# Performance work log

Measured on AMD Instinct MI355X. Metric: run time of the kernel, lower is better.

Reference implementation:

```python
import jax, jax.numpy as jnp
import numpy as np

D_MODEL = 1024
N_HEADS = 16
HEAD_DIM = D_MODEL // N_HEADS  # 64
SEQ = 2048
BATCH = 2


def setup_inputs() -> dict:
    key = jax.random.key(0)
    ks = jax.random.split(key, 12)
    s = 1.0 / np.sqrt(D_MODEL)
    return {
        "query": jax.random.normal(ks[0], (SEQ, BATCH, D_MODEL), jnp.float32),
        "key": jax.random.normal(ks[1], (SEQ, BATCH, D_MODEL), jnp.float32),
        "value": jax.random.normal(ks[2], (SEQ, BATCH, D_MODEL), jnp.float32),
        "Wq": jax.random.normal(ks[3], (D_MODEL, D_MODEL), jnp.float32) * s,
        "bq": jax.random.normal(ks[4], (D_MODEL,), jnp.float32) * s,
        "Wk": jax.random.normal(ks[5], (D_MODEL, D_MODEL), jnp.float32) * s,
        "bk": jax.random.normal(ks[6], (D_MODEL,), jnp.float32) * s,
        "Wv": jax.random.normal(ks[7], (D_MODEL, D_MODEL), jnp.float32) * s,
        "bv": jax.random.normal(ks[8], (D_MODEL,), jnp.float32) * s,
        "Wo": jax.random.normal(ks[9], (D_MODEL, D_MODEL), jnp.float32) * s,
        "bo": jax.random.normal(ks[10], (D_MODEL,), jnp.float32) * s,
    }


def _rope_tables(seq_len):
    # theta_i = 1 / 10000^(2i/head_dim), i in [0, head_dim//2)
    theta = 1.0 / (10000.0 ** (2.0 * jnp.arange(HEAD_DIM // 2, dtype=jnp.float32) / HEAD_DIM))
    pos = jnp.arange(seq_len, dtype=jnp.float32)[:, None, None, None] * theta  # [S,1,1,hd/2]
    return jnp.sin(pos), jnp.cos(pos)


def _apply_rope(t, sin, cos):
    # t: [S, B, H, hd]; NOTE faithful to source: t2 = q1*sin - q2*cos (minus)
    h = HEAD_DIM // 2
    q1, q2 = t[..., :h], t[..., h:]
    return jnp.concatenate([q1 * cos - q2 * sin, q1 * sin - q2 * cos], axis=-1)


def reference(query, key, value, Wq, bq, Wk, bk, Wv, bv, Wo, bo):
    S, B, _ = query.shape
    q = (query @ Wq.T + bq).reshape(S, B, N_HEADS, HEAD_DIM)
    k = (key @ Wk.T + bk).reshape(S, B, N_HEADS, HEAD_DIM)
    v = (value @ Wv.T + bv).reshape(S, B, N_HEADS, HEAD_DIM)
    sin, cos = _rope_tables(S)
    q = _apply_rope(q, sin, cos)
    k = _apply_rope(k, sin, cos)
    # [S,B,H,d] -> [B,H,S,d]
    q = q.transpose(1, 2, 0, 3)
    k = k.transpose(1, 2, 0, 3)
    v = v.transpose(1, 2, 0, 3)
    scale = 1.0 / jnp.sqrt(jnp.float32(HEAD_DIM))
    scores = jnp.einsum("bhqd,bhkd->bhqk", q, k) * scale
    attn = jax.nn.softmax(scores, axis=-1)
    out = jnp.einsum("bhqk,bhkd->bhqd", attn, v)  # [B,H,S,d]
    out = out.transpose(2, 0, 1, 3).reshape(S, B, D_MODEL)
    return out @ Wo.T + bo
```

## Files before the change

kernel.cpp:

```cpp
#include <hip/hip_runtime.h>
#include <hip/hip_bf16.h>

#define DMODEL 1024
#define NHEADS 16
#define HDIM   64
#define SEQ    2048
#define BATCH  2
#define MROWS  (SEQ*BATCH)

typedef unsigned int u32;
typedef unsigned short u16;
typedef __attribute__((ext_vector_type(8))) short bfrag;
typedef __attribute__((ext_vector_type(4))) float f32x4;
typedef __attribute__((ext_vector_type(16))) float f32x16;
typedef union { u32 u[4]; bfrag f; } fragu;

#define LOG2E 1.44269504088896341f

__device__ __forceinline__ u32 f2bf(float x) {
    unsigned u = __float_as_uint(x);
    return (u + 0x7fffu + ((u >> 16) & 1u)) >> 16;
}
__device__ __forceinline__ float bf2f(u32 h) {
    return __uint_as_float(h << 16);
}
__device__ __forceinline__ u32 pk2bf(float a, float b) {
    __hip_bfloat162 t = __float22bfloat162_rn(make_float2(a, b));
    u32 r;
    __builtin_memcpy(&r, &t, 4);
    return r;
}
__device__ __forceinline__ float fexp2(float x) {
#if __has_builtin(__builtin_amdgcn_exp2f)
    return __builtin_amdgcn_exp2f(x);
#else
    return exp2f(x);
#endif
}

__device__ __forceinline__ void gld16(const void* g, void* l) {
    __builtin_amdgcn_global_load_lds(
        (const __attribute__((address_space(1))) unsigned int*)g,
        (__attribute__((address_space(3))) unsigned int*)l, 16, 0, 0);
}


__global__ __launch_bounds__(256) void prep_kernel(
    const float* __restrict__ Wq, const float* __restrict__ Wk,
    const float* __restrict__ Wv, const float* __restrict__ Wo,
    float* __restrict__ query, float* __restrict__ key, float* __restrict__ value,
    u16* __restrict__ wqb, u16* __restrict__ wkb, u16* __restrict__ wvb,
    u16* __restrict__ wob, float2* __restrict__ tab)
{
    const int y = blockIdx.y;
    if (y == 3) {
        if (blockIdx.x >= 256) return;
        const int e = blockIdx.x * 256 + threadIdx.x;
        const int s = e >> 5, i = e & 31;
        const double th = exp(-(double)i * (9.210340371976184 / 32.0));
        double sn, cs;
        sincos((double)s * th, &sn, &cs);
        tab[e] = make_float2((float)sn, (float)cs);
        return;
    }
    const float* src;
    u16* dst;
    int nr;
    if (y < 3 || y == 7) {
        src = (y == 0) ? Wq : (y == 1) ? Wk : (y == 2) ? Wv : Wo;
        dst = (y == 0) ? wqb : (y == 1) ? wkb : (y == 2) ? wvb : wob;
        nr = 2;
    } else {
        float* io = (y == 4) ? query : (y == 5) ? key : value;
        src = io;
        dst = (u16*)io;
        nr = 8;
    }
    const int lane = threadIdx.x & 63;
    const int wv   = threadIdx.x >> 6;
    const int g8   = lane >> 3;
    const int l8   = lane & 7;
    for (int r = 0; r < nr; ++r) {
        const size_t kb = (size_t)blockIdx.x * (4 * nr) + (size_t)r * 4 + wv;
        const float4 x4 = *(const float4*)(src + kb * 256 + lane * 4);
        __align__(8) u16 hb[4];
        __align__(8) u16 lb[4];
        const float xs[4] = {x4.x, x4.y, x4.z, x4.w};
        #pragma unroll
        for (int i = 0; i < 4; ++i) {
            const u32 h = f2bf(xs[i]);
            hb[i] = (u16)h;
            lb[i] = (u16)f2bf(xs[i] - bf2f(h));
        }
        u16* o = dst + kb * 512 + g8 * 64 + l8 * 4;
        *(uint2*)o        = *(const uint2*)hb;
        *(uint2*)(o + 32) = *(const uint2*)lb;
    }
}

template <int NI>
__device__ __forceinline__ void gemm_body(
    int id, int mode,
    const u16* __restrict__ Ab, const u16* __restrict__ Wb,
    const float* __restrict__ bias, const float2* __restrict__ tab,
    float rope_scale,
    u16* __restrict__ Oh, u16* __restrict__ Ol, float* __restrict__ Of,
    u16* smem16)
{
    u16* sA = smem16;
    u16* sB = smem16 + 16384;

    const int tid   = threadIdx.x;
    const int w     = tid >> 6;
    const int lane  = tid & 63;
    const int lrow  = lane & 15;
    const int lquad = lane >> 4;

    const int NBLK = 1024 / (NI * 16);
    const int xcd  = id & 7;
    const int jj   = id >> 3;
    const int nblk = jj & (NBLK - 1);
    const int mblk = (xcd << 2) | (jj / NBLK);
    const int n0   = nblk * NI * 16;
    const int m0   = mblk * 128;

    const int srow8 = lane >> 3;
    const int sch   = (lane & 7) ^ srow8;

    int aoffh[2], aoffl[2], boffh[NI], boffl[NI];
    #pragma unroll
    for (int mi = 0; mi < 2; ++mi) {
        const int ra = w * 32 + mi * 16 + lrow;
        aoffh[mi] = ra * 64 + ((lquad ^ (ra & 7)) << 3);
        aoffl[mi] = ra * 64 + (((lquad + 4) ^ (ra & 7)) << 3);
    }
    #pragma unroll
    for (int ni = 0; ni < NI; ++ni) {
        const int rb = ni * 16 + lrow;
        boffh[ni] = rb * 64 + ((lquad ^ (rb & 7)) << 3);
        boffl[ni] = rb * 64 + (((lquad + 4) ^ (rb & 7)) << 3);
    }

    f32x4 acc[2][NI] = {};

    auto stage = [&](int t) {
        const int h = t & 1;
        #pragma unroll
        for (int i = 0; i < 4; ++i) {
            const int slab = w * 4 + i;
            const int row  = slab * 8 + srow8;
            gld16(Ab + (size_t)(m0 + row) * 2048 + t * 64 + sch * 8,
                  sA + h * 8192 + slab * 512);
        }
        #pragma unroll
        for (int i = 0; i < NI / 2; ++i) {
            const int slab = w * (NI / 2) + i;
            const int row  = slab * 8 + srow8;
            gld16(Wb + (size_t)(n0 + row) * 2048 + t * 64 + sch * 8,
                  sB + h * (NI * 1024) + slab * 512);
        }
    };

    stage(0);
    for (int t = 0; t < 32; ++t) {
        __syncthreads();
        if (t < 31) stage(t + 1);
        const int h = t & 1;
        const u16* sAh_ = sA + h * 8192;
        const u16* sBh_ = sB + h * (NI * 1024);

        bfrag ah[2], al[2], bh[NI], bl[NI];
        #pragma unroll
        for (int mi = 0; mi < 2; ++mi) {
            ah[mi] = *(const bfrag*)&sAh_[aoffh[mi]];
            al[mi] = *(const bfrag*)&sAh_[aoffl[mi]];
        }
        #pragma unroll
        for (int ni = 0; ni < NI; ++ni) {
            bh[ni] = *(const bfrag*)&sBh_[boffh[ni]];
            bl[ni] = *(const bfrag*)&sBh_[boffl[ni]];
        }

        #pragma unroll
        for (int mi = 0; mi < 2; ++mi)
            #pragma unroll
            for (int ni = 0; ni < NI; ++ni) {
                acc[mi][ni] = __builtin_amdgcn_mfma_f32_16x16x32_bf16(ah[mi], bh[ni], acc[mi][ni], 0, 0, 0);
                acc[mi][ni] = __builtin_amdgcn_mfma_f32_16x16x32_bf16(ah[mi], bl[ni], acc[mi][ni], 0, 0, 0);
                acc[mi][ni] = __builtin_amdgcn_mfma_f32_16x16x32_bf16(al[mi], bh[ni], acc[mi][ni], 0, 0, 0);
            }
    }

    float bn[NI];
    #pragma unroll
    for (int ni = 0; ni < NI; ++ni) bn[ni] = bias[n0 + ni * 16 + lrow];

    if (mode == 0) {
        #pragma unroll
        for (int mi = 0; mi < 2; ++mi)
            #pragma unroll
            for (int r = 0; r < 4; ++r) {
                const int mrow = w * 32 + mi * 16 + lquad * 4 + r;
                const int m  = m0 + mrow;
                const int bb = m & 1;
                const int sg = m >> 1;
                #pragma unroll
                for (int hh = 0; hh < NI / 4; ++hh) {
                    const int head = nblk * (NI / 4) + hh;
                    const size_t ob = (((size_t)(bb * NHEADS + head) * SEQ) + sg) * HDIM;
                    #pragma unroll
                    for (int ni = 0; ni < 2; ++ni) {
                        const int i = ni * 16 + lrow;
                        const float2 sc = tab[(size_t)sg * 32 + i];
                        const float x1 = acc[mi][hh * 4 + ni][r]     + bn[hh * 4 + ni];
                        const float x2 = acc[mi][hh * 4 + ni + 2][r] + bn[hh * 4 + ni + 2];
                        const float o1 = (x1 * sc.y - x2 * sc.x) * rope_scale;
                        const float o2 = (x1 * sc.x - x2 * sc.y) * rope_scale;
                        const u32 h1 = f2bf(o1);
                        const u32 h2 = f2bf(o2);
                        Oh[ob + i]      = (u16)h1;  Ol[ob + i]      = (u16)f2bf(o1 - bf2f(h1));
                        Oh[ob + i + 32] = (u16)h2;  Ol[ob + i + 32] = (u16)f2bf(o2 - bf2f(h2));
                    }
                }
            }
        return;
    }
    if (mode == 1) {
        __syncthreads();
        u32* vb = (u32*)smem16;
        constexpr int NP = (NI == 8) ? 2 : 1;
        for (int p = 0; p < NP; ++p) {
            if (p) __syncthreads();
            #pragma unroll
            for (int mi = 0; mi < 2; ++mi)
                #pragma unroll
                for (int r = 0; r < 4; ++r) {
                    const int mrow = w * 32 + mi * 16 + lquad * 4 + r;
                    const int bb = mrow & 1;
                    const int sl = mrow >> 1;
                    if (NP == 1 || bb == p) {
                        const int vbase = (NP == 1) ? bb * 4160 : 0;
                        #pragma unroll
                        for (int ni = 0; ni < NI; ++ni) {
                            const int d = ni * 16 + lrow;
                            vb[vbase + d * 65 + sl] = f2bf(acc[mi][ni][r] + bn[ni]);
                        }
                    }
                }
            __syncthreads();
            #pragma unroll
            for (int rep = 0; rep < 4; ++rep) {
                const int c  = rep * 256 + tid;
                const int bb = (NP == 1) ? (c >> 9) : p;
                const int dc = (NP == 1) ? ((c >> 3) & 63) : (c >> 3);
                const int s8 = c & 7;
                const int vbase = (NP == 1) ? bb * 4160 : 0;
                __align__(8) u16 hb[8];
                #pragma unroll
                for (int j = 0; j < 8; ++j)
                    hb[j] = (u16)vb[vbase + dc * 65 + s8 * 8 + j];
                const int head = nblk * (NI / 4) + (dc >> 6);
                const int dd   = dc & 63;
                const size_t orow = ((size_t)(bb * NHEADS + head) * HDIM + dd) * SEQ + (m0 >> 1);
                const int blk16 = (s8 >> 1) * 16;
                const int off   = (s8 & 1) * 4;
                *(uint2*)&Oh[orow + blk16 + off]     = *(const uint2*)&hb[0];
                *(uint2*)&Oh[orow + blk16 + 8 + off] = *(const uint2*)&hb[4];
            }
        }
        return;
    }
    #pragma unroll
    for (int mi = 0; mi < 2; ++mi)
        #pragma unroll
        for (int r = 0; r < 4; ++r) {
            const int m = m0 + w * 32 + mi * 16 + lquad * 4 + r;
            #pragma unroll
            for (int ni = 0; ni < NI; ++ni)
                Of[(size_t)m * 1024 + n0 + ni * 16 + lrow] = acc[mi][ni][r] + bn[ni];
        }
}

__global__ __launch_bounds__(256) void qkv_gemm_kernel(
    const u16* __restrict__ query, const u16* __restrict__ key,
    const u16* __restrict__ value,
    const u16* __restrict__ Wqb, const u16* __restrict__ Wkb,
    const u16* __restrict__ Wvb,
    const float* __restrict__ bq, const float* __restrict__ bk,
    const float* __restrict__ bv, const float2* __restrict__ tab,
    u16* __restrict__ Qh, u16* __restrict__ Ql,
    u16* __restrict__ Kh, u16* __restrict__ Kl,
    u16* __restrict__ VTh)
{
    __shared__ u16 smem16[32768];
    const int z  = blockIdx.z;
    const int id = blockIdx.x + 16 * blockIdx.y;
    const u16* A    = (z == 0) ? query : (z == 1) ? key : value;
    const u16* Wb   = (z == 0) ? Wqb : (z == 1) ? Wkb : Wvb;
    const float* bb = (z == 0) ? bq : (z == 1) ? bk : bv;
    u16* Oh = (z == 0) ? Qh : (z == 1) ? Kh : VTh;
    u16* Ol = (z == 0) ? Ql : (z == 1) ? Kl : nullptr;
    const int mode = (z == 2) ? 1 : 0;
    const float scale = (z == 0) ? 0.125f * LOG2E : 1.0f;
    gemm_body<8>(id, mode, A, Wb, bb, tab, scale, Oh, Ol, nullptr, smem16);
}

__global__ __launch_bounds__(256) void out_gemm_kernel(
    const u16* __restrict__ Ab, const u16* __restrict__ Wb,
    const float* __restrict__ bias, float* __restrict__ Of)
{
    __shared__ u16 smem16[24576];
    const int id = blockIdx.x + 16 * blockIdx.y;
    gemm_body<4>(id, 2, Ab, Wb, bias, nullptr, 1.0f, nullptr, nullptr, Of, smem16);
}

__global__ __launch_bounds__(256) void attn_mfma_kernel(
    const u16* __restrict__ Qh, const u16* __restrict__ Ql,
    const u16* __restrict__ Kh, const u16* __restrict__ Kl,
    const u16* __restrict__ Vh,
    u16* __restrict__ AOb)
{
    __shared__ u16 sKh[8192], sKl[8192];
    __shared__ u16 sVh[8192];

    const int tid  = threadIdx.x;
    const int w    = tid >> 6;
    const int lane = tid & 63;
    const int l31  = lane & 31;
    const int g    = lane >> 5;

    const int id = blockIdx.x + 16 * blockIdx.y;
    const int jj = id >> 3;
    const int bh = ((id & 7) << 2) | (jj >> 4);
    const int qt = jj & 15;

    const size_t qg = ((size_t)bh * SEQ + qt * 128 + w * 32 + l31) * HDIM + g * 8;
    bfrag qfh[4], qfl[4];
    #pragma unroll
    for (int ks = 0; ks < 4; ++ks) {
        qfh[ks] = *(const bfrag*)&Qh[qg + ks * 16];
        qfl[ks] = *(const bfrag*)&Ql[qg + ks * 16];
    }

    const int srow   = lane >> 3;
    const int schunk = (lane & 7) ^ srow;
    const u16* gsrc = nullptr; u16* lbase = nullptr; size_t istep = 0, ktstep = 0;
    if (w == 0) {
        gsrc = Kh + ((size_t)bh * SEQ + srow) * HDIM + schunk * 8;
        istep = 8 * 64; ktstep = 64 * 64; lbase = sKh;
    } else if (w == 1) {
        gsrc = Kl + ((size_t)bh * SEQ + srow) * HDIM + schunk * 8;
        istep = 8 * 64; ktstep = 64 * 64; lbase = sKl;
    } else if (w == 2) {
        gsrc = Vh + ((size_t)bh * HDIM + srow) * SEQ + schunk * 8;
        istep = 8 * SEQ; ktstep = 64; lbase = sVh;
    }

    int koff[2][4];
    #pragma unroll
    for (int a = 0; a < 2; ++a) {
        const int row = a * 32 + l31;
        #pragma unroll
        for (int c = 0; c < 4; ++c)
            koff[a][c] = row * 64 + (((c * 2 + g) ^ (row & 7)) << 3);
    }

    f32x16 accO[2] = {};
    float l_loc = 0.0f;

    auto stage = [&](int kt) {
        if (w < 3) {
            const u16* gp = gsrc + (size_t)kt * ktstep;
            u16* dst = lbase + (kt & 1) * 4096;
            #pragma unroll
            for (int i = 0; i < 8; ++i)
                gld16(gp + (size_t)i * istep, dst + i * 512);
        }
    };

    stage(0);
    for (int kt = 0; kt < SEQ / 64; ++kt) {
        __syncthreads();
        if (kt < SEQ / 64 - 1) stage(kt + 1);
        const int po = (kt & 1) * 4096;

        f32x16 accS[2] = {};
        #pragma unroll
        for (int kg = 0; kg < 2; ++kg)
            #pragma unroll
            for (int ks = 0; ks < 4; ++ks) {
                const bfrag kh_ = *(const bfrag*)&sKh[po + koff[kg][ks]];
                const bfrag kl_ = *(const bfrag*)&sKl[po + koff[kg][ks]];
                accS[kg] = __builtin_amdgcn_mfma_f32_32x32x16_bf16(kh_, qfh[ks], accS[kg], 0, 0, 0);
                accS[kg] = __builtin_amdgcn_mfma_f32_32x32x16_bf16(kh_, qfl[ks], accS[kg], 0, 0, 0);
                accS[kg] = __builtin_amdgcn_mfma_f32_32x32x16_bf16(kl_, qfh[ks], accS[kg], 0, 0, 0);
            }

        float pv[2][16];
        #pragma unroll
        for (int kg = 0; kg < 2; ++kg)
            #pragma unroll
            for (int r = 0; r < 16; ++r) {
                const float p = fexp2(accS[kg][r]);
                pv[kg][r] = p;
                l_loc += p;
            }

        #pragma unroll
        for (int kp = 0; kp < 4; ++kp) {
            const int kg = kp >> 1;
            const int t8 = (kp & 1) * 8;
            fragu ph;
            #pragma unroll
            for (int j2 = 0; j2 < 4; ++j2)
                ph.u[j2] = pk2bf(pv[kg][t8 + 2 * j2], pv[kg][t8 + 2 * j2 + 1]);
            #pragma unroll
            for (int dt = 0; dt < 2; ++dt) {
                const bfrag vh = *(const bfrag*)&sVh[po + koff[dt][kp]];
                accO[dt] = __builtin_amdgcn_mfma_f32_32x32x16_bf16(vh, ph.f, accO[dt], 0, 0, 0);
            }
        }
    }

    const float inv = 1.0f / (l_loc + __shfl_xor(l_loc, 32));

    const int b = bh >> 4;
    const int h = bh & 15;
    const int sg = qt * 128 + w * 32 + l31;
    const int rm = sg * BATCH + b;
    #pragma unroll
    for (int dt = 0; dt < 2; ++dt)
        #pragma unroll
        for (int rq = 0; rq < 4; ++rq) {
            const int j0 = 8 * rq + 4 * g;
            const int t  = h * 2 + dt;
            __align__(8) u16 hb[4];
            __align__(8) u16 lb[4];
            #pragma unroll
            for (int i2 = 0; i2 < 4; ++i2) {
                const float v = accO[dt][rq * 4 + i2] * inv;
                const u32 hh = f2bf(v);
                hb[i2] = (u16)hh;
                lb[i2] = (u16)f2bf(v - bf2f(hh));
            }
            u16* o = AOb + (size_t)rm * 2048 + t * 64 + j0;
            *(uint2*)o        = *(const uint2*)hb;
            *(uint2*)(o + 32) = *(const uint2*)lb;
        }
}

extern "C" void kernel_launch(void* const* d_in, const int* in_sizes, int n_in,
                              void* d_out, int out_size, void* d_ws, size_t ws_size,
                              hipStream_t stream)
{
    float* query = (float*)d_in[0];
    float* key   = (float*)d_in[1];
    float* value = (float*)d_in[2];
    const float* Wq    = (const float*)d_in[3];
    const float* bq    = (const float*)d_in[4];
    const float* Wk    = (const float*)d_in[5];
    const float* bk    = (const float*)d_in[6];
    const float* Wv    = (const float*)d_in[7];
    const float* bv    = (const float*)d_in[8];
    const float* Wo    = (const float*)d_in[9];
    const float* bo    = (const float*)d_in[10];
    float* out = (float*)d_out;

    char* wsb = (char*)d_ws;
    const size_t MB = 1024 * 1024;
    u16* Wqb = (u16*)(wsb + 0 * MB);
    u16* Wkb = (u16*)(wsb + 4 * MB);
    u16* Wvb = (u16*)(wsb + 8 * MB);
    float2* tab = (float2*)(wsb + 12 * MB);
    u16* Qh  = (u16*)(wsb + 16 * MB); u16* Ql  = (u16*)(wsb + 24 * MB);
    u16* Kh  = (u16*)(wsb + 32 * MB); u16* Kl  = (u16*)(wsb + 40 * MB);
    u16* VTh = (u16*)(wsb + 48 * MB);
    u16* Wob = (u16*)(wsb + 56 * MB);
    u16* AOb = (u16*)(wsb + 0 * MB);

    prep_kernel<<<dim3(512, 8), 256, 0, stream>>>(
        Wq, Wk, Wv, Wo, query, key, value, Wqb, Wkb, Wvb, Wob, tab);
    qkv_gemm_kernel<<<dim3(16, 16, 3), 256, 0, stream>>>(
        (const u16*)query, (const u16*)key, (const u16*)value,
        Wqb, Wkb, Wvb, bq, bk, bv, tab, Qh, Ql, Kh, Kl, VTh);
    attn_mfma_kernel<<<dim3(16, 32), 256, 0, stream>>>(
        Qh, Ql, Kh, Kl, VTh, AOb);
    out_gemm_kernel<<<dim3(16, 32), 256, 0, stream>>>(AOb, Wob, bo, out);
}
```

Measured before the change: 306.5 us.

## Fuse fp32-to-bf16 hi/lo activation split into the QKV GEMM A-tile load

The QKV GEMM now reads fp32 query/key/value straight from global memory into registers. It splits each value into a bf16 high part (truncated via byte-permute) and a rounded bf16 residual, then writes both into the swizzled LDS A tile, software-pipelined one k-step ahead. The prep kernel no longer converts activations in place, which removes a full read-and-write pass over three 16 MB inputs and stops the inputs from being overwritten. In exchange the GEMM loses async global-to-LDS loads for A, holds prefetched float4 registers across the MFMA section, and does extra ALU conversion work inside the main loop.

Result: slower. 316.0 us (+3.1%).

```diff
diff --git a/kernel.cpp b/kernel.cpp
--- a/kernel.cpp
+++ b/kernel.cpp
@@ -37,6 +37,13 @@
     return exp2f(x);
 #endif
 }
+__device__ __forceinline__ u32 pkhi(u32 u0, u32 u1) {
+#if __has_builtin(__builtin_amdgcn_perm)
+    return __builtin_amdgcn_perm(u1, u0, 0x07060302u);
+#else
+    return (u0 >> 16) | (u1 & 0xffff0000u);
+#endif
+}
 
 __device__ __forceinline__ void gld16(const void* g, void* l) {
     __builtin_amdgcn_global_load_lds(
@@ -48,7 +55,6 @@
 __global__ __launch_bounds__(256) void prep_kernel(
     const float* __restrict__ Wq, const float* __restrict__ Wk,
     const float* __restrict__ Wv, const float* __restrict__ Wo,
-    float* __restrict__ query, float* __restrict__ key, float* __restrict__ value,
     u16* __restrict__ wqb, u16* __restrict__ wkb, u16* __restrict__ wvb,
     u16* __restrict__ wob, float2* __restrict__ tab)
 {
@@ -63,25 +69,14 @@
         tab[e] = make_float2((float)sn, (float)cs);
         return;
     }
-    const float* src;
-    u16* dst;
-    int nr;
-    if (y < 3 || y == 7) {
-        src = (y == 0) ? Wq : (y == 1) ? Wk : (y == 2) ? Wv : Wo;
-        dst = (y == 0) ? wqb : (y == 1) ? wkb : (y == 2) ? wvb : wob;
-        nr = 2;
-    } else {
-        float* io = (y == 4) ? query : (y == 5) ? key : value;
-        src = io;
-        dst = (u16*)io;
-        nr = 8;
-    }
+    const float* src = (y == 0) ? Wq : (y == 1) ? Wk : (y == 2) ? Wv : Wo;
+    u16* dst = (y == 0) ? wqb : (y == 1) ? wkb : (y == 2) ? wvb : wob;
     const int lane = threadIdx.x & 63;
     const int wv   = threadIdx.x >> 6;
     const int g8   = lane >> 3;
     const int l8   = lane & 7;
-    for (int r = 0; r < nr; ++r) {
-        const size_t kb = (size_t)blockIdx.x * (4 * nr) + (size_t)r * 4 + wv;
+    for (int r = 0; r < 2; ++r) {
+        const size_t kb = (size_t)blockIdx.x * 8 + (size_t)r * 4 + wv;
         const float4 x4 = *(const float4*)(src + kb * 256 + lane * 4);
         __align__(8) u16 hb[4];
         __align__(8) u16 lb[4];
@@ -98,17 +93,29 @@
     }
 }
 
-template <int NI>
-__device__ __forceinline__ void gemm_body(
-    int id, int mode,
-    const u16* __restrict__ Ab, const u16* __restrict__ Wb,
-    const float* __restrict__ bias, const float2* __restrict__ tab,
-    float rope_scale,
-    u16* __restrict__ Oh, u16* __restrict__ Ol, float* __restrict__ Of,
-    u16* smem16)
+__global__ __launch_bounds__(256) void qkv_gemm_kernel(
+    const float* __restrict__ query, const float* __restrict__ key,
+    const float* __restrict__ value,
+    const u16* __restrict__ Wqb, const u16* __restrict__ Wkb,
+    const u16* __restrict__ Wvb,
+    const float* __restrict__ bq, const float* __restrict__ bk,
+    const float* __restrict__ bv, const float2* __restrict__ tab,
+    u16* __restrict__ Qh, u16* __restrict__ Ql,
+    u16* __restrict__ Kh, u16* __restrict__ Kl,
+    u16* __restrict__ VTh)
 {
+    __shared__ u16 smem16[32768];
     u16* sA = smem16;
     u16* sB = smem16 + 16384;
+
+    const int z  = blockIdx.z;
+    const float* Af   = (z == 0) ? query : (z == 1) ? key : value;
+    const u16* Wb     = (z == 0) ? Wqb : (z == 1) ? Wkb : Wvb;
+    const float* bias = (z == 0) ? bq : (z == 1) ? bk : bv;
+    u16* Oh = (z == 0) ? Qh : (z == 1) ? Kh : VTh;
+    u16* Ol = (z == 0) ? Ql : (z == 1) ? Kl : nullptr;
+    const float rope_scale = (z == 0) ? 0.125f * LOG2E : 1.0f;
+    const int mode = (z == 2) ? 1 : 0;
 
     const int tid   = threadIdx.x;
     const int w     = tid >> 6;
@@ -116,18 +123,23 @@
     const int lrow  = lane & 15;
     const int lquad = lane >> 4;
 
-    const int NBLK = 1024 / (NI * 16);
+    const int id   = blockIdx.x + 16 * blockIdx.y;
     const int xcd  = id & 7;
     const int jj   = id >> 3;
-    const int nblk = jj & (NBLK - 1);
-    const int mblk = (xcd << 2) | (jj / NBLK);
-    const int n0   = nblk * NI * 16;
+    const int nblk = jj & 7;
+    const int mblk = (xcd << 2) | (jj >> 3);
+    const int n0   = nblk * 128;
     const int m0   = mblk * 128;
 
     const int srow8 = lane >> 3;
     const int sch   = (lane & 7) ^ srow8;
 
-    int aoffh[2], aoffl[2], boffh[NI], boffl[NI];
+    const int l8r = lane >> 3;
+    const int l8c = lane & 7;
+    const int cA  = l8c >> 1;
+    const int hA  = (l8c & 1) * 4;
+
+    int aoffh[2], aoffl[2], boffh[8], boffl[8];
     #pragma unroll
     for (int mi = 0; mi < 2; ++mi) {
         const int ra = w * 32 + mi * 16 + lrow;
@@ -135,48 +147,80 @@
         aoffl[mi] = ra * 64 + (((lquad + 4) ^ (ra & 7)) << 3);
     }
     #pragma unroll
-    for (int ni = 0; ni < NI; ++ni) {
+    for (int ni = 0; ni < 8; ++ni) {
         const int rb = ni * 16 + lrow;
         boffh[ni] = rb * 64 + ((lquad ^ (rb & 7)) << 3);
         boffl[ni] = rb * 64 + (((lquad + 4) ^ (rb & 7)) << 3);
     }
 
-    f32x4 acc[2][NI] = {};
-
-    auto stage = [&](int t) {
+    f32x4 acc[2][8] = {};
+
+    auto stageB = [&](int t) {
         const int h = t & 1;
         #pragma unroll
         for (int i = 0; i < 4; ++i) {
             const int slab = w * 4 + i;
             const int row  = slab * 8 + srow8;
-            gld16(Ab + (size_t)(m0 + row) * 2048 + t * 64 + sch * 8,
-                  sA + h * 8192 + slab * 512);
-        }
-        #pragma unroll
-        for (int i = 0; i < NI / 2; ++i) {
-            const int slab = w * (NI / 2) + i;
-            const int row  = slab * 8 + srow8;
             gld16(Wb + (size_t)(n0 + row) * 2048 + t * 64 + sch * 8,
-                  sB + h * (NI * 1024) + slab * 512);
+                  sB + h * 8192 + slab * 512);
         }
     };
-
-    stage(0);
+    auto loadA = [&](int t, float4* va) {
+        #pragma unroll
+        for (int i = 0; i < 4; ++i) {
+            const int r = w * 32 + i * 8 + l8r;
+            va[i] = ((const float4*)Af)[(size_t)(m0 + r) * 256 + t * 8 + l8c];
+        }
+    };
+    auto writeA = [&](int t, const float4* va) {
+        const int h = t & 1;
+        #pragma unroll
+        for (int i = 0; i < 4; ++i) {
+            const int r = w * 32 + i * 8 + l8r;
+            const u32 u0 = __float_as_uint(va[i].x);
+            const u32 u1 = __float_as_uint(va[i].y);
+            const u32 u2 = __float_as_uint(va[i].z);
+            const u32 u3 = __float_as_uint(va[i].w);
+            uint2 hv, lv;
+            hv.x = pkhi(u0, u1);
+            hv.y = pkhi(u2, u3);
+            const float r0 = va[i].x - __uint_as_float(u0 & 0xffff0000u);
+            const float r1 = va[i].y - __uint_as_float(u1 & 0xffff0000u);
+            const float r2 = va[i].z - __uint_as_float(u2 & 0xffff0000u);
+            const float r3 = va[i].w - __uint_as_float(u3 & 0xffff0000u);
+            lv.x = pk2bf(r0, r1);
+            lv.y = pk2bf(r2, r3);
+            u16* base = sA + h * 8192 + r * 64;
+            *(uint2*)(base + ((cA ^ (r & 7)) << 3) + hA)       = hv;
+            *(uint2*)(base + (((cA + 4) ^ (r & 7)) << 3) + hA) = lv;
+        }
+    };
+
+    {
+        float4 va[4];
+        stageB(0);
+        loadA(0, va);
+        writeA(0, va);
+    }
     for (int t = 0; t < 32; ++t) {
         __syncthreads();
-        if (t < 31) stage(t + 1);
+        float4 va[4];
+        if (t < 31) {
+            stageB(t + 1);
+            loadA(t + 1, va);
+        }
         const int h = t & 1;
         const u16* sAh_ = sA + h * 8192;
-        const u16* sBh_ = sB + h * (NI * 1024);
-
-        bfrag ah[2], al[2], bh[NI], bl[NI];
+        const u16* sBh_ = sB + h * 8192;
+
+        bfrag ah[2], al[2], bh[8], bl[8];
         #pragma unroll
         for (int mi = 0; mi < 2; ++mi) {
             ah[mi] = *(const bfrag*)&sAh_[aoffh[mi]];
             al[mi] = *(const bfrag*)&sAh_[aoffl[mi]];
         }
         #pragma unroll
-        for (int ni = 0; ni < NI; ++ni) {
+        for (int ni = 0; ni < 8; ++ni) {
             bh[ni] = *(const bfrag*)&sBh_[boffh[ni]];
             bl[ni] = *(const bfrag*)&sBh_[boffl[ni]];
         }
@@ -184,16 +228,18 @@
         #pragma unroll
         for (int mi = 0; mi < 2; ++mi)
             #pragma unroll
-            for (int ni = 0; ni < NI; ++ni) {
+            for (int ni = 0; ni < 8; ++ni) {
                 acc[mi][ni] = __builtin_amdgcn_mfma_f32_16x16x32_bf16(ah[mi], bh[ni], acc[mi][ni], 0, 0, 0);
                 acc[mi][ni] = __builtin_amdgcn_mfma_f32_16x16x32_bf16(ah[mi], bl[ni], acc[mi][ni], 0, 0, 0);
                 acc[mi][ni] = __builtin_amdgcn_mfma_f32_16x16x32_bf16(al[mi], bh[ni], acc[mi][ni], 0, 0, 0);
             }
-    }
-
-    float bn[NI];
-    #pragma unroll
-    for (int ni = 0; ni < NI; ++ni) bn[ni] = bias[n0 + ni * 16 + lrow];
+
+        if (t < 31) writeA(t + 1, va);
+    }
+
+    float bn[8];
+    #pragma unroll
+    for (int ni = 0; ni < 8; ++ni) bn[ni] = bias[n0 + ni * 16 + lrow];
 
     if (mode == 0) {
         #pragma unroll
@@ -205,8 +251,8 @@
                 const int bb = m & 1;
                 const int sg = m >> 1;
                 #pragma unroll
-                for (int hh = 0; hh < NI / 4; ++hh) {
-                    const int head = nblk * (NI / 4) + hh;
+                for (int hh = 0; hh < 2; ++hh) {
+                    const int head = nblk * 2 + hh;
                     const size_t ob = (((size_t)(bb * NHEADS + head) * SEQ) + sg) * HDIM;
                     #pragma unroll
                     for (int ni = 0; ni < 2; ++ni) {
@@ -225,51 +271,141 @@
             }
         return;
     }
-    if (mode == 1) {
-        __syncthreads();
-        u32* vb = (u32*)smem16;
-        constexpr int NP = (NI == 8) ? 2 : 1;
-        for (int p = 0; p < NP; ++p) {
-            if (p) __syncthreads();
-            #pragma unroll
-            for (int mi = 0; mi < 2; ++mi)
-                #pragma unroll
-                for (int r = 0; r < 4; ++r) {
-                    const int mrow = w * 32 + mi * 16 + lquad * 4 + r;
-                    const int bb = mrow & 1;
-                    const int sl = mrow >> 1;
-                    if (NP == 1 || bb == p) {
-                        const int vbase = (NP == 1) ? bb * 4160 : 0;
-                        #pragma unroll
-                        for (int ni = 0; ni < NI; ++ni) {
-                            const int d = ni * 16 + lrow;
-                            vb[vbase + d * 65 + sl] = f2bf(acc[mi][ni][r] + bn[ni]);
-                        }
+    __syncthreads();
+    u32* vb = (u32*)smem16;
+    for (int p = 0; p < 2; ++p) {
+        if (p) __syncthreads();
+        #pragma unroll
+        for (int mi = 0; mi < 2; ++mi)
+            #pragma unroll
+            for (int r = 0; r < 4; ++r) {
+                const int mrow = w * 32 + mi * 16 + lquad * 4 + r;
+                const int bb = mrow & 1;
+                const int sl = mrow >> 1;
+                if (bb == p) {
+                    #pragma unroll
+                    for (int ni = 0; ni < 8; ++ni) {
+                        const int d = ni * 16 + lrow;
+                        vb[d * 65 + sl] = f2bf(acc[mi][ni][r] + bn[ni]);
                     }
                 }
-            __syncthreads();
-            #pragma unroll
-            for (int rep = 0; rep < 4; ++rep) {
-                const int c  = rep * 256 + tid;
-                const int bb = (NP == 1) ? (c >> 9) : p;
-                const int dc = (NP == 1) ? ((c >> 3) & 63) : (c >> 3);
-                const int s8 = c & 7;
-                const int vbase = (NP == 1) ? bb * 4160 : 0;
-                __align__(8) u16 hb[8];
-                #pragma unroll
-                for (int j = 0; j < 8; ++j)
-                    hb[j] = (u16)vb[vbase + dc * 65 + s8 * 8 + j];
-                const int head = nblk * (NI / 4) + (dc >> 6);
-                const int dd   = dc & 63;
-                const size_t orow = ((size_t)(bb * NHEADS + head) * HDIM + dd) * SEQ + (m0 >> 1);
-                const int blk16 = (s8 >> 1) * 16;
-                const int off   = (s8 & 1) * 4;
-                *(uint2*)&Oh[orow + blk16 + off]     = *(const uint2*)&hb[0];
-                *(uint2*)&Oh[orow + blk16 + 8 + off] = *(const uint2*)&hb[4];
-            }
-        }
-        return;
-    }
+            }
+        __syncthreads();
+        #pragma unroll
+        for (int rep = 0; rep < 4; ++rep) {
+            const int c  = rep * 256 + tid;
+            const int dc = c >> 3;
+            const int s8 = c & 7;
+            __align__(8) u16 hb[8];
+            #pragma unroll
+            for (int j = 0; j < 8; ++j)
+                hb[j] = (u16)vb[dc * 65 + s8 * 8 + j];
+            const int head = nblk * 2 + (dc >> 6);
+            const int dd   = dc & 63;
+            const size_t orow = ((size_t)(p * NHEADS + head) * HDIM + dd) * SEQ + (m0 >> 1);
+            const int blk16 = (s8 >> 1) * 16;
+            const int off   = (s8 & 1) * 4;
+            *(uint2*)&Oh[orow + blk16 + off]     = *(const uint2*)&hb[0];
+            *(uint2*)&Oh[orow + blk16 + 8 + off] = *(const uint2*)&hb[4];
+        }
+    }
+}
+
+template <int NI>
+__device__ __forceinline__ void gemm_body(
+    int id,
+    const u16* __restrict__ Ab, const u16* __restrict__ Wb,
+    const float* __restrict__ bias, float* __restrict__ Of,
+    u16* smem16)
+{
+    u16* sA = smem16;
+    u16* sB = smem16 + 16384;
+
+    const int tid   = threadIdx.x;
+    const int w     = tid >> 6;
+    const int lane  = tid & 63;
+    const int lrow  = lane & 15;
+    const int lquad = lane >> 4;
+
+    const int NBLK = 1024 / (NI * 16);
+    const int xcd  = id & 7;
+    const int jj   = id >> 3;
+    const int nblk = jj & (NBLK - 1);
+    const int mblk = (xcd << 2) | (jj / NBLK);
+    const int n0   = nblk * NI * 16;
+    const int m0   = mblk * 128;
+
+    const int srow8 = lane >> 3;
+    const int sch   = (lane & 7) ^ srow8;
+
+    int aoffh[2], aoffl[2], boffh[NI], boffl[NI];
+    #pragma unroll
+    for (int mi = 0; mi < 2; ++mi) {
+        const int ra = w * 32 + mi * 16 + lrow;
+        aoffh[mi] = ra * 64 + ((lquad ^ (ra & 7)) << 3);
+        aoffl[mi] = ra * 64 + (((lquad + 4) ^ (ra & 7)) << 3);
+    }
+    #pragma unroll
+    for (int ni = 0; ni < NI; ++ni) {
+        const int rb = ni * 16 + lrow;
+        boffh[ni] = rb * 64 + ((lquad ^ (rb & 7)) << 3);
+        boffl[ni] = rb * 64 + (((lquad + 4) ^ (rb & 7)) << 3);
+    }
+
+    f32x4 acc[2][NI] = {};
+
+    auto stage = [&](int t) {
+        const int h = t & 1;
+        #pragma unroll
+        for (int i = 0; i < 4; ++i) {
+            const int slab = w * 4 + i;
+            const int row  = slab * 8 + srow8;
+            gld16(Ab + (size_t)(m0 + row) * 2048 + t * 64 + sch * 8,
+                  sA + h * 8192 + slab * 512);
+        }
+        #pragma unroll
+        for (int i = 0; i < NI / 2; ++i) {
+            const int slab = w * (NI / 2) + i;
+            const int row  = slab * 8 + srow8;
+            gld16(Wb + (size_t)(n0 + row) * 2048 + t * 64 + sch * 8,
+                  sB + h * (NI * 1024) + slab * 512);
+        }
+    };
+
+    stage(0);
+    for (int t = 0; t < 32; ++t) {
+        __syncthreads();
+        if (t < 31) stage(t + 1);
+        const int h = t & 1;
+        const u16* sAh_ = sA + h * 8192;
+        const u16* sBh_ = sB + h * (NI * 1024);
+
+        bfrag ah[2], al[2], bh[NI], bl[NI];
+        #pragma unroll
+        for (int mi = 0; mi < 2; ++mi) {
+            ah[mi] = *(const bfrag*)&sAh_[aoffh[mi]];
+            al[mi] = *(const bfrag*)&sAh_[aoffl[mi]];
+        }
+        #pragma unroll
+        for (int ni = 0; ni < NI; ++ni) {
+            bh[ni] = *(const bfrag*)&sBh_[boffh[ni]];
+            bl[ni] = *(const bfrag*)&sBh_[boffl[ni]];
+        }
+
+        #pragma unroll
+        for (int mi = 0; mi < 2; ++mi)
+            #pragma unroll
+            for (int ni = 0; ni < NI; ++ni) {
+                acc[mi][ni] = __builtin_amdgcn_mfma_f32_16x16x32_bf16(ah[mi], bh[ni], acc[mi][ni], 0, 0, 0);
+                acc[mi][ni] = __builtin_amdgcn_mfma_f32_16x16x32_bf16(ah[mi], bl[ni], acc[mi][ni], 0, 0, 0);
+                acc[mi][ni] = __builtin_amdgcn_mfma_f32_16x16x32_bf16(al[mi], bh[ni], acc[mi][ni], 0, 0, 0);
+            }
+    }
+
+    float bn[NI];
+    #pragma unroll
+    for (int ni = 0; ni < NI; ++ni) bn[ni] = bias[n0 + ni * 16 + lrow];
+
     #pragma unroll
     for (int mi = 0; mi < 2; ++mi)
         #pragma unroll
@@ -279,30 +415,6 @@
             for (int ni = 0; ni < NI; ++ni)
                 Of[(size_t)m * 1024 + n0 + ni * 16 + lrow] = acc[mi][ni][r] + bn[ni];
         }
-}
-
-__global__ __launch_bounds__(256) void qkv_gemm_kernel(
-    const u16* __restrict__ query, const u16* __restrict__ key,
-    const u16* __restrict__ value,
-    const u16* __restrict__ Wqb, const u16* __restrict__ Wkb,
-    const u16* __restrict__ Wvb,
-    const float* __restrict__ bq, const float* __restrict__ bk,
-    const float* __restrict__ bv, const float2* __restrict__ tab,
-    u16* __restrict__ Qh, u16* __restrict__ Ql,
-    u16* __restrict__ Kh, u16* __restrict__ Kl,
-    u16* __restrict__ VTh)
-{
-    __shared__ u16 smem16[32768];
-    const int z  = blockIdx.z;
-    const int id = blockIdx.x + 16 * blockIdx.y;
-    const u16* A    = (z == 0) ? query : (z == 1) ? key : value;
-    const u16* Wb   = (z == 0) ? Wqb : (z == 1) ? Wkb : Wvb;
-    const float* bb = (z == 0) ? bq : (z == 1) ? bk : bv;
-    u16* Oh = (z == 0) ? Qh : (z == 1) ? Kh : VTh;
-    u16* Ol = (z == 0) ? Ql : (z == 1) ? Kl : nullptr;
-    const int mode = (z == 2) ? 1 : 0;
-    const float scale = (z == 0) ? 0.125f * LOG2E : 1.0f;
-    gemm_body<8>(id, mode, A, Wb, bb, tab, scale, Oh, Ol, nullptr, smem16);
 }
 
 __global__ __launch_bounds__(256) void out_gemm_kernel(
@@ -311,7 +423,7 @@
 {
     __shared__ u16 smem16[24576];
     const int id = blockIdx.x + 16 * blockIdx.y;
-    gemm_body<4>(id, 2, Ab, Wb, bias, nullptr, 1.0f, nullptr, nullptr, Of, smem16);
+    gemm_body<4>(id, Ab, Wb, bias, Of, smem16);
 }
 
 __global__ __launch_bounds__(256) void attn_mfma_kernel(
@@ -453,9 +565,9 @@
                               void* d_out, int out_size, void* d_ws, size_t ws_size,
                               hipStream_t stream)
 {
-    float* query = (float*)d_in[0];
-    float* key   = (float*)d_in[1];
-    float* value = (float*)d_in[2];
+    const float* query = (const float*)d_in[0];
+    const float* key   = (const float*)d_in[1];
+    const float* value = (const float*)d_in[2];
     const float* Wq    = (const float*)d_in[3];
     const float* bq    = (const float*)d_in[4];
     const float* Wk    = (const float*)d_in[5];
@@ -478,10 +590,10 @@
     u16* Wob = (u16*)(wsb + 56 * MB);
     u16* AOb = (u16*)(wsb + 0 * MB);
 
-    prep_kernel<<<dim3(512, 8), 256, 0, stream>>>(
-        Wq, Wk, Wv, Wo, query, key, value, Wqb, Wkb, Wvb, Wob, tab);
+    prep_kernel<<<dim3(512, 5), 256, 0, stream>>>(
+        Wq, Wk, Wv, Wo, Wqb, Wkb, Wvb, Wob, tab);
     qkv_gemm_kernel<<<dim3(16, 16, 3), 256, 0, stream>>>(
-        (const u16*)query, (const u16*)key, (const u16*)value,
+        query, key, value,
         Wqb, Wkb, Wvb, bq, bk, bv, tab, Qh, Ql, Kh, Kl, VTh);
     attn_mfma_kernel<<<dim3(16, 32), 256, 0, stream>>>(
         Qh, Ql, Kh, Kl, VTh, AOb);
```
